# Optimization experiments

Measured on AMD Instinct MI355X. Metric: run time of the kernel, lower is better.

The kernel has to match this reference:

```python
import jax, jax.numpy as jnp
import numpy as np

B, S, D, H = 8, 256, 16, 256
NH, DH, L = 8, H // 8, 3
H2, H4, FF = H // 2, H // 4, 2 * H


def _ln(x, g, b, eps=1e-5):
    m = jnp.mean(x, axis=-1, keepdims=True)
    v = jnp.var(x, axis=-1, keepdims=True)
    return (x - m) / jnp.sqrt(v + eps) * g + b


def setup_inputs() -> dict:
    key = jax.random.key(0)
    ks = iter(jax.random.split(key, 32))
    w = lambda *sh: jax.random.normal(next(ks), sh, jnp.float32) * 0.05
    inp = {
        'parts': jax.random.normal(next(ks), (B, S, D), jnp.float32),
        'target_sequence': jax.random.randint(next(ks), (B, S), 0, S),
        # part encoder
        'W_pe1': w(H2, D), 'b_pe1': jnp.zeros((H2,)),
        'W_pe2': w(H2, H2), 'b_pe2': jnp.zeros((H2,)),
        'pos_emb': w(S, H4),
        # transformer encoder (3 layers, stacked)
        'Wqkv': w(L, 3 * H, H), 'bqkv': jnp.zeros((L, 3 * H)),
        'Wo': w(L, H, H), 'bo': jnp.zeros((L, H)),
        'ln1_g': jnp.ones((L, H)), 'ln1_b': jnp.zeros((L, H)),
        'W1f': w(L, FF, H), 'b1f': jnp.zeros((L, FF)),
        'W2f': w(L, H, FF), 'b2f': jnp.zeros((L, H)),
        'ln2_g': jnp.ones((L, H)), 'ln2_b': jnp.zeros((L, H)),
        # LSTM decoder
        'Wih': w(4 * H, H), 'Whh': w(4 * H, H),
        'bih': jnp.zeros((4 * H,)), 'bhh': jnp.zeros((4 * H,)),
        # pointer
        'Wp': w(H, H), 'bp': jnp.zeros((H,)), 'v_ptr': w(H),
    }
    return inp


def reference(parts, target_sequence, W_pe1, b_pe1, W_pe2, b_pe2, pos_emb,
              Wqkv, bqkv, Wo, bo, ln1_g, ln1_b, W1f, b1f, W2f, b2f, ln2_g, ln2_b,
              Wih, Whh, bih, bhh, Wp, bp, v_ptr):
    Bk, Sk = parts.shape[:2]
    # ---- encode_inputs (dropout inactive in eval) ----
    pe = jax.nn.relu(parts @ W_pe1.T + b_pe1) @ W_pe2.T + b_pe2          # [B,S,H/2]
    pos = jnp.broadcast_to(pos_emb[None, :Sk], (Bk, Sk, H4))              # [B,S,H/4]
    pad = jnp.zeros((Bk, Sk, H - H2 - H4), parts.dtype)
    x = jnp.concatenate([pe, pos, pad], axis=-1)                          # [B,S,H]
    scale = 1.0 / np.sqrt(DH)
    for l in range(L):  # post-norm transformer encoder layers
        qkv = x @ Wqkv[l].T + bqkv[l]
        q, k, v = jnp.split(qkv, 3, axis=-1)
        q = q.reshape(Bk, Sk, NH, DH)
        k = k.reshape(Bk, Sk, NH, DH)
        v = v.reshape(Bk, Sk, NH, DH)
        att = jax.nn.softmax(jnp.einsum('bqhd,bkhd->bhqk', q, k) * scale, axis=-1)
        o = jnp.einsum('bhqk,bkhd->bqhd', att, v).reshape(Bk, Sk, H)
        o = o @ Wo[l].T + bo[l]
        x = _ln(x + o, ln1_g[l], ln1_b[l])
        f = jax.nn.relu(x @ W1f[l].T + b1f[l]) @ W2f[l].T + b2f[l]
        x = _ln(x + f, ln2_g[l], ln2_b[l])
    enc = x                                                               # [B,S,H]
    # ---- teacher-forced LSTM decode (teacher_forcing_ratio=1.0) ----
    gathered = jnp.take_along_axis(enc, target_sequence[:, :, None], axis=1)  # [B,T,H]
    dec_in = jnp.concatenate([jnp.zeros((Bk, 1, H), enc.dtype), gathered[:, :-1]], 1)
    dec_in = dec_in.transpose(1, 0, 2)                                    # [T,B,H]

    def step(carry, xt):
        h, c = carry
        g = xt @ Wih.T + bih + h @ Whh.T + bhh
        i, f, gg, o = jnp.split(g, 4, axis=-1)
        c = jax.nn.sigmoid(f) * c + jax.nn.sigmoid(i) * jnp.tanh(gg)
        h = jax.nn.sigmoid(o) * jnp.tanh(c)
        return (h, c), h

    h0 = jnp.zeros((Bk, H), enc.dtype)
    _, dec_out = jax.lax.scan(step, (h0, h0), dec_in)
    dec_out = dec_out.transpose(1, 0, 2)                                  # [B,T,H]
    # ---- pointer logits: v . tanh(Wp d_t + Wp e_i), batched over (t,i) ----
    pd = dec_out @ Wp.T + bp                                              # [B,T,H]
    pen = enc @ Wp.T + bp                                                 # [B,S,H]
    logits = jnp.tanh(pd[:, :, None, :] + pen[:, None, :, :]) @ v_ptr     # [B,T,S]
    return logits
```

## Files before the change

kernel.cpp:

```cpp
#include <hip/hip_runtime.h>
#include <cstdint>
#include <cstddef>


typedef _Float16 h2 __attribute__((ext_vector_type(2)));
typedef short bf16x8 __attribute__((ext_vector_type(8)));
typedef float f32x4 __attribute__((ext_vector_type(4)));

__device__ __forceinline__ float sigf(float x) { return 1.0f / (1.0f + __expf(-x)); }
__device__ __forceinline__ float tanhfast(float x) {
  float e = __expf(-2.0f * fabsf(x));
  float t = (1.0f - e) / (1.0f + e);
  return copysignf(t, x);
}
__device__ __forceinline__ h2 cvt2(float a, float b) {
  h2 r; r.x = (_Float16)a; r.y = (_Float16)b; return r;
}
__device__ __forceinline__ h2 bch2(unsigned int u) { return __builtin_bit_cast(h2, u); }
__device__ __forceinline__ unsigned int bcu(h2 v) { return __builtin_bit_cast(unsigned int, v); }
__device__ __forceinline__ unsigned short f2bf(float f) {
  unsigned int u = __float_as_uint(f);
  u = (u + 0x7fffu + ((u >> 16) & 1u)) >> 16;
  return (unsigned short)u;
}

__device__ __forceinline__ float fdot2f(h2 a, h2 b, float c) {
#if __has_builtin(__builtin_amdgcn_fdot2)
  return __builtin_amdgcn_fdot2(a, b, c, false);
#else
  return fmaf((float)a.x, (float)b.x, fmaf((float)a.y, (float)b.y, c));
#endif
}

__global__ void convert_all(const float* __restrict__ s0, ushort* __restrict__ d0,
                            const float* __restrict__ s1, ushort* __restrict__ d1,
                            const float* __restrict__ s2, ushort* __restrict__ d2,
                            const float* __restrict__ s3, ushort* __restrict__ d3,
                            const float* __restrict__ s4, ushort* __restrict__ d4,
                            const float* __restrict__ s5, ushort* __restrict__ d5) {
  int i = blockIdx.x * 256 + threadIdx.x;
  if (i < 589824) { d0[i] = f2bf(s0[i]); return; }
  i -= 589824;
  if (i < 196608) { d1[i] = f2bf(s1[i]); return; }
  i -= 196608;
  if (i < 393216) { d2[i] = f2bf(s2[i]); return; }
  i -= 393216;
  if (i < 393216) { d3[i] = f2bf(s3[i]); return; }
  i -= 393216;
  if (i < 262144) { d4[i] = f2bf(s4[i]); return; }
  i -= 262144;
  if (i < 65536) d5[i] = f2bf(s5[i]);
}

__global__ void part_encoder(const float* __restrict__ parts, const float* __restrict__ Wpe1,
                             const float* __restrict__ bpe1, const float* __restrict__ Wpe2,
                             const float* __restrict__ bpe2, const float* __restrict__ pos,
                             float* __restrict__ x, ushort* __restrict__ xb) {
  __shared__ float prow[16];
  __shared__ float pe1[128];
  int row = blockIdx.x;
  int s = row & 255;
  int tid = threadIdx.x;
  if (tid < 16) prow[tid] = parts[row * 16 + tid];
  __syncthreads();
  float a = bpe1[tid];
#pragma unroll
  for (int k = 0; k < 16; ++k) a = fmaf(prow[k], Wpe1[tid * 16 + k], a);
  pe1[tid] = fmaxf(a, 0.0f);
  __syncthreads();
  float a2 = bpe2[tid];
  for (int k = 0; k < 128; ++k) a2 = fmaf(pe1[k], Wpe2[tid * 128 + k], a2);
  x[(size_t)row * 256 + tid] = a2;
  xb[(size_t)row * 256 + tid] = f2bf(a2);
  if (tid < 64) {
    float p = pos[s * 64 + tid];
    x[(size_t)row * 256 + 128 + tid] = p;
    xb[(size_t)row * 256 + 128 + tid] = f2bf(p);
    x[(size_t)row * 256 + 192 + tid] = 0.0f;
    xb[(size_t)row * 256 + 192 + tid] = 0;
  }
}

template <int ACT, int OUT>
__global__ __launch_bounds__(64) void gemm_bf16(
    const ushort* __restrict__ A, const ushort* __restrict__ Wt,
    const float* __restrict__ bias1, const float* __restrict__ bias2,
    void* __restrict__ Cout, int N, int K) {
  int lane = threadIdx.x;
  int m0 = blockIdx.y * 16;
  int n0 = blockIdx.x * 64;
  int r15 = lane & 15;
  int kg = lane >> 4;
  f32x4 acc0 = {0.f, 0.f, 0.f, 0.f}, acc1 = acc0, acc2 = acc0, acc3 = acc0;
  const ushort* arow = A + (size_t)(m0 + r15) * K + kg * 8;
  const ushort* w0 = Wt + (size_t)(n0 + r15) * K + kg * 8;
  const ushort* w1 = w0 + (size_t)16 * K;
  const ushort* w2 = w0 + (size_t)32 * K;
  const ushort* w3 = w0 + (size_t)48 * K;
  for (int k0 = 0; k0 < K; k0 += 32) {
    bf16x8 af = *(const bf16x8*)(arow + k0);
    bf16x8 b0 = *(const bf16x8*)(w0 + k0);
    bf16x8 b1 = *(const bf16x8*)(w1 + k0);
    bf16x8 b2 = *(const bf16x8*)(w2 + k0);
    bf16x8 b3 = *(const bf16x8*)(w3 + k0);
    acc0 = __builtin_amdgcn_mfma_f32_16x16x32_bf16(af, b0, acc0, 0, 0, 0);
    acc1 = __builtin_amdgcn_mfma_f32_16x16x32_bf16(af, b1, acc1, 0, 0, 0);
    acc2 = __builtin_amdgcn_mfma_f32_16x16x32_bf16(af, b2, acc2, 0, 0, 0);
    acc3 = __builtin_amdgcn_mfma_f32_16x16x32_bf16(af, b3, acc3, 0, 0, 0);
  }
#pragma unroll
  for (int nn = 0; nn < 4; ++nn) {
    f32x4 a = (nn == 0) ? acc0 : (nn == 1) ? acc1 : (nn == 2) ? acc2 : acc3;
    int n = n0 + nn * 16 + r15;
    float bsum = bias1[n] + (bias2 ? bias2[n] : 0.0f);
    if (OUT == 3) {
      int b = m0 >> 8;
      int mloc = (m0 & 255) + kg * 4;
      float4 o4 = {a[0] + bsum, a[1] + bsum, a[2] + bsum, a[3] + bsum};
      *(float4*)&((float*)Cout)[((size_t)(b * 256 + n)) * 256 + mloc] = o4;
    } else {
#pragma unroll
      for (int r = 0; r < 4; ++r) {
        int m = m0 + kg * 4 + r;
        float v = a[r] + bsum;
        if (ACT == 1) v = fmaxf(v, 0.0f);
        if (OUT == 1)
          ((ushort*)Cout)[(size_t)m * N + n] = f2bf(v);
        else
          ((float*)Cout)[(size_t)m * N + n] = v;
      }
    }
  }
}

__global__ void attn_kernel(const float* __restrict__ qkv, ushort* __restrict__ attout) {
  extern __shared__ float sm[];
  float* kl = sm;
  float* ql = sm + 256 * 33;
  float* sc = sm + 256 * 33 + 32 * 33;
  int qt = blockIdx.x, h = blockIdx.y, b = blockIdx.z;
  int tid = threadIdx.x;
  {
    int j = tid;
    const float* src = qkv + (size_t)(b * 256 + j) * 768 + 256 + h * 32;
#pragma unroll
    for (int d = 0; d < 32; d += 4) {
      float4 v = *(const float4*)(src + d);
      kl[j * 33 + d] = v.x; kl[j * 33 + d + 1] = v.y; kl[j * 33 + d + 2] = v.z; kl[j * 33 + d + 3] = v.w;
    }
  }
  {
    int i = tid >> 3, d4 = (tid & 7) * 4;
    const float* src = qkv + (size_t)(b * 256 + qt * 32 + i) * 768 + h * 32;
    float4 v = *(const float4*)(src + d4);
    ql[i * 33 + d4] = v.x; ql[i * 33 + d4 + 1] = v.y; ql[i * 33 + d4 + 2] = v.z; ql[i * 33 + d4 + 3] = v.w;
  }
  __syncthreads();
  int i = tid >> 3, c = tid & 7;
  const float scale = 0.17677669529663687f;
  float sv[32];
  float mx = -1e30f;
  for (int jj = 0; jj < 32; ++jj) {
    int j = jj * 8 + c;
    float s = 0.0f;
#pragma unroll
    for (int d = 0; d < 32; ++d) s = fmaf(ql[i * 33 + d], kl[j * 33 + d], s);
    s *= scale;
    sv[jj] = s;
    mx = fmaxf(mx, s);
  }
  mx = fmaxf(mx, __shfl_xor(mx, 1));
  mx = fmaxf(mx, __shfl_xor(mx, 2));
  mx = fmaxf(mx, __shfl_xor(mx, 4));
  float sum = 0.0f;
  for (int jj = 0; jj < 32; ++jj) {
    float p = __expf(sv[jj] - mx);
    sc[i * 257 + jj * 8 + c] = p;
    sum += p;
  }
  sum += __shfl_xor(sum, 1);
  sum += __shfl_xor(sum, 2);
  sum += __shfl_xor(sum, 4);
  float inv = 1.0f / sum;
  __syncthreads();
  float a0 = 0, a1 = 0, a2 = 0, a3 = 0;
  int d0 = c * 4;
  const float* vbase = qkv + 512 + h * 32 + d0;
  for (int j = 0; j < 256; ++j) {
    float p = sc[i * 257 + j];
    float4 v = *(const float4*)(vbase + (size_t)(b * 256 + j) * 768);
    a0 = fmaf(p, v.x, a0); a1 = fmaf(p, v.y, a1); a2 = fmaf(p, v.z, a2); a3 = fmaf(p, v.w, a3);
  }
  int orow = b * 256 + qt * 32 + i;
  ushort4 o4;
  o4.x = f2bf(a0 * inv); o4.y = f2bf(a1 * inv); o4.z = f2bf(a2 * inv); o4.w = f2bf(a3 * inv);
  *(ushort4*)&attout[(size_t)orow * 256 + h * 32 + d0] = o4;
}

__global__ void ln_residual(float* __restrict__ x, const float* __restrict__ o,
                            const float* __restrict__ g, const float* __restrict__ bt,
                            ushort* __restrict__ xb) {
  int row = blockIdx.x, tid = threadIdx.x;
  float e = x[(size_t)row * 256 + tid] + o[(size_t)row * 256 + tid];
  float s = e, q = e * e;
#pragma unroll
  for (int off = 32; off >= 1; off >>= 1) {
    s += __shfl_xor(s, off);
    q += __shfl_xor(q, off);
  }
  __shared__ float ps[4], pq[4];
  int wid = tid >> 6, lane = tid & 63;
  if (lane == 0) { ps[wid] = s; pq[wid] = q; }
  __syncthreads();
  float St = ps[0] + ps[1] + ps[2] + ps[3];
  float Qt = pq[0] + pq[1] + pq[2] + pq[3];
  float mean = St * (1.0f / 256.0f);
  float var = Qt * (1.0f / 256.0f) - mean * mean;
  float y = (e - mean) * rsqrtf(var + 1e-5f) * g[tid] + bt[tid];
  x[(size_t)row * 256 + tid] = y;
  xb[(size_t)row * 256 + tid] = f2bf(y);
}

__global__ void gather_dec_in(const ushort* __restrict__ encb, const int* __restrict__ ts,
                              ushort* __restrict__ dec_in) {
  int bx = blockIdx.x;
  int t = bx >> 3, b = bx & 7;
  int tid = threadIdx.x;
  ushort4 v = {0, 0, 0, 0};
  if (t > 0) {
    int sidx = ts[b * 256 + t - 1];
    v = *(const ushort4*)&encb[((size_t)(b * 256 + sidx)) * 256 + tid * 4];
  }
  *(ushort4*)&dec_in[(size_t)bx * 256 + tid * 4] = v;
}

__global__ __attribute__((amdgpu_flat_work_group_size(512, 512), amdgpu_waves_per_eu(1, 1)))
void lstm_scan512(const float* __restrict__ Xw, const float* __restrict__ Whh,
                  ushort* __restrict__ dec_out) {
  extern __shared__ char smem[];
  uint4* wlds = (uint4*)smem;
  h2* hbuf = (h2*)(smem + 131072);
  int b = blockIdx.x;
  int t0 = threadIdx.x;
  int u = t0 >> 1, p = t0 & 1;
  int rA = u + 256 * p;
  int rB = u + 512 + 256 * p;

  h2 w0[96], w1[96];
  {
    const float4* sA = (const float4*)(Whh + (size_t)rA * 256);
    const float4* sB = (const float4*)(Whh + (size_t)rB * 256);
#pragma unroll
    for (int k = 0; k < 48; ++k) {
      float4 v = sA[k];
      w0[2 * k] = cvt2(v.x, v.y);
      w0[2 * k + 1] = cvt2(v.z, v.w);
    }
#pragma unroll
    for (int k = 0; k < 48; ++k) {
      float4 v = sB[k];
      w1[2 * k] = cvt2(v.x, v.y);
      w1[2 * k + 1] = cvt2(v.z, v.w);
    }
#pragma unroll
    for (int qc = 0; qc < 8; ++qc) {
      float4 vA0 = sA[48 + 2 * qc], vA1 = sA[48 + 2 * qc + 1];
      float4 vB0 = sB[48 + 2 * qc], vB1 = sB[48 + 2 * qc + 1];
      uint4 uA, uB;
      uA.x = bcu(cvt2(vA0.x, vA0.y)); uA.y = bcu(cvt2(vA0.z, vA0.w));
      uA.z = bcu(cvt2(vA1.x, vA1.y)); uA.w = bcu(cvt2(vA1.z, vA1.w));
      uB.x = bcu(cvt2(vB0.x, vB0.y)); uB.y = bcu(cvt2(vB0.z, vB0.w));
      uB.z = bcu(cvt2(vB1.x, vB1.y)); uB.w = bcu(cvt2(vB1.z, vB1.w));
      wlds[qc * 1024 + rA] = uA;
      wlds[qc * 1024 + rB] = uB;
    }
  }
  if (t0 < 128) ((uint4*)hbuf)[t0 & 63] = make_uint4(0, 0, 0, 0);
  float c = 0.0f;
  float xnA = Xw[(size_t)b * 1024 + rA];
  float xnB = Xw[(size_t)b * 1024 + rB];
  __syncthreads();

  for (int t = 0; t < 256; ++t) {
    float xwA = xnA, xwB = xnB;
    if (t < 255) {
      const float* xp = Xw + (size_t)((t + 1) * 8 + b) * 1024;
      xnA = xp[rA]; xnB = xp[rB];
    }
    const uint4* hb = (const uint4*)(hbuf + (size_t)(t & 1) * 128);
    float a0 = 0.0f, a1 = 0.0f;
#pragma unroll
    for (int q = 0; q < 24; ++q) {
      uint4 hv = hb[q];
      h2 hx = bch2(hv.x), hy = bch2(hv.y), hz = bch2(hv.z), hw = bch2(hv.w);
      a0 = fdot2f(w0[4 * q], hx, a0); a0 = fdot2f(w0[4 * q + 1], hy, a0);
      a0 = fdot2f(w0[4 * q + 2], hz, a0); a0 = fdot2f(w0[4 * q + 3], hw, a0);
      a1 = fdot2f(w1[4 * q], hx, a1); a1 = fdot2f(w1[4 * q + 1], hy, a1);
      a1 = fdot2f(w1[4 * q + 2], hz, a1); a1 = fdot2f(w1[4 * q + 3], hw, a1);
    }
#pragma unroll
    for (int qc = 0; qc < 8; ++qc) {
      uint4 hv = hb[24 + qc];
      h2 hx = bch2(hv.x), hy = bch2(hv.y), hz = bch2(hv.z), hw = bch2(hv.w);
      uint4 uA = wlds[qc * 1024 + rA];
      uint4 uB = wlds[qc * 1024 + rB];
      a0 = fdot2f(bch2(uA.x), hx, a0); a0 = fdot2f(bch2(uA.y), hy, a0);
      a0 = fdot2f(bch2(uA.z), hz, a0); a0 = fdot2f(bch2(uA.w), hw, a0);
      a1 = fdot2f(bch2(uB.x), hx, a1); a1 = fdot2f(bch2(uB.y), hy, a1);
      a1 = fdot2f(bch2(uB.z), hz, a1); a1 = fdot2f(bch2(uB.w), hw, a1);
    }
    a0 += xwA;
    a1 += xwB;
    float ev = sigf(a0) * tanhfast(a1);
    float ep = __shfl_xor(ev, 1);
    if (p == 1) {
      c = sigf(a0) * c + ep;
      float hv_ = sigf(a1) * tanhfast(c);
      ((_Float16*)(hbuf + (size_t)((t + 1) & 1) * 128))[u] = (_Float16)hv_;
      dec_out[((size_t)(b * 256 + t)) * 256 + u] = f2bf(hv_);
    }
    __syncthreads();
  }
}

__global__ void pointer_kernel(const float* __restrict__ pd, const float* __restrict__ penT,
                               const float* __restrict__ vptr, float* __restrict__ out) {
  __shared__ float pdr[256];
  __shared__ float vl[256];
  int bx = blockIdx.x;
  int b = bx >> 8;
  int tid = threadIdx.x;
  pdr[tid] = pd[(size_t)bx * 256 + tid];
  vl[tid] = vptr[tid];
  __syncthreads();
  const float* pT = penT + (size_t)b * 256 * 256;
  float acc = 0.0f;
  for (int h = 0; h < 256; ++h) {
    acc = fmaf(vl[h], tanhfast(pdr[h] + pT[(size_t)h * 256 + tid]), acc);
  }
  out[(size_t)bx * 256 + tid] = acc;
}

extern "C" void kernel_launch(void* const* d_in, const int* in_sizes, int n_in,
                              void* d_out, int out_size, void* d_ws, size_t ws_size,
                              hipStream_t stream) {
  const float* parts = (const float*)d_in[0];
  const int* ts = (const int*)d_in[1];
  const float* Wpe1 = (const float*)d_in[2];
  const float* bpe1 = (const float*)d_in[3];
  const float* Wpe2 = (const float*)d_in[4];
  const float* bpe2 = (const float*)d_in[5];
  const float* pos = (const float*)d_in[6];
  const float* Wqkv = (const float*)d_in[7];
  const float* bqkv = (const float*)d_in[8];
  const float* Wo = (const float*)d_in[9];
  const float* bo = (const float*)d_in[10];
  const float* ln1g = (const float*)d_in[11];
  const float* ln1b = (const float*)d_in[12];
  const float* W1f = (const float*)d_in[13];
  const float* b1f = (const float*)d_in[14];
  const float* W2f = (const float*)d_in[15];
  const float* b2f = (const float*)d_in[16];
  const float* ln2g = (const float*)d_in[17];
  const float* ln2b = (const float*)d_in[18];
  const float* Wih = (const float*)d_in[19];
  const float* Whh = (const float*)d_in[20];
  const float* bih = (const float*)d_in[21];
  const float* bhh = (const float*)d_in[22];
  const float* Wp = (const float*)d_in[23];
  const float* bp = (const float*)d_in[24];
  const float* vptr = (const float*)d_in[25];
  float* out = (float*)d_out;

  float* W = (float*)d_ws;
  float* xbuf = W;
  ushort* xbf = (ushort*)(W + 524288);
  float* SCR = W + 786432;
  float* qkvb = SCR;
  float* obuf = SCR + 1572864;
  float* Xw = SCR;
  float* pdb = SCR;
  float* penTb = SCR + 1048576;
  ushort* attbf = (ushort*)(W + 2883584);
  ushort* ffbf = (ushort*)(W + 3145728);
  ushort* dec_inbf = (ushort*)(W + 3145728);
  ushort* dec_outbf = (ushort*)(W + 3407872);
  ushort* wqkvbf = (ushort*)(W + 3670016);
  ushort* wobf   = (ushort*)(W + 3964928);
  ushort* w1fbf  = (ushort*)(W + 4063232);
  ushort* w2fbf  = (ushort*)(W + 4259840);
  ushort* wihbf  = (ushort*)(W + 4456448);
  ushort* wpbf   = (ushort*)(W + 4587520);

  const int attnLDS = (256 * 33 + 32 * 33 + 32 * 257) * 4;
  const int scan512LDS = 131072 + 1024;
  hipFuncSetAttribute((const void*)attn_kernel, hipFuncAttributeMaxDynamicSharedMemorySize, attnLDS);
  hipFuncSetAttribute((const void*)lstm_scan512, hipFuncAttributeMaxDynamicSharedMemorySize, scan512LDS);

  convert_all<<<7424, 256, 0, stream>>>(Wqkv, wqkvbf, Wo, wobf, W1f, w1fbf,
                                        W2f, w2fbf, Wih, wihbf, Wp, wpbf);

  part_encoder<<<2048, 128, 0, stream>>>(parts, Wpe1, bpe1, Wpe2, bpe2, pos, xbuf, xbf);
  for (int l = 0; l < 3; ++l) {
    gemm_bf16<0, 0><<<dim3(12, 128), 64, 0, stream>>>(xbf, wqkvbf + (size_t)l * 196608,
                                                      bqkv + l * 768, nullptr, qkvb, 768, 256);
    attn_kernel<<<dim3(8, 8, 8), 256, attnLDS, stream>>>(qkvb, attbf);
    gemm_bf16<0, 0><<<dim3(4, 128), 64, 0, stream>>>(attbf, wobf + (size_t)l * 65536,
                                                     bo + l * 256, nullptr, obuf, 256, 256);
    ln_residual<<<2048, 256, 0, stream>>>(xbuf, obuf, ln1g + l * 256, ln1b + l * 256, xbf);
    gemm_bf16<1, 1><<<dim3(8, 128), 64, 0, stream>>>(xbf, w1fbf + (size_t)l * 131072,
                                                     b1f + l * 512, nullptr, ffbf, 512, 256);
    gemm_bf16<0, 0><<<dim3(4, 128), 64, 0, stream>>>(ffbf, w2fbf + (size_t)l * 131072,
                                                     b2f + l * 256, nullptr, obuf, 256, 512);
    ln_residual<<<2048, 256, 0, stream>>>(xbuf, obuf, ln2g + l * 256, ln2b + l * 256, xbf);
  }
  gather_dec_in<<<2048, 64, 0, stream>>>(xbf, ts, dec_inbf);
  gemm_bf16<0, 0><<<dim3(16, 128), 64, 0, stream>>>(dec_inbf, wihbf, bih, bhh, Xw, 1024, 256);
  lstm_scan512<<<8, 512, scan512LDS, stream>>>(Xw, Whh, dec_outbf);
  gemm_bf16<0, 0><<<dim3(4, 128), 64, 0, stream>>>(dec_outbf, wpbf, bp, nullptr, pdb, 256, 256);
  gemm_bf16<0, 3><<<dim3(4, 128), 64, 0, stream>>>(xbf, wpbf, bp, nullptr, penTb, 256, 256);
  pointer_kernel<<<2048, 256, 0, stream>>>(pdb, penTb, vptr, out);
}
```

Baseline: 825.5 us.

## Fuse residual LayerNorm into output GEMMs and gather into LSTM input GEMM

Adds a gemm_ln kernel in which four waves compute a full 16x256 output tile, stage it in shared memory, then apply the residual add and LayerNorm before writing fp32 and bf16 activations. This replaces the separate Wo/W2f GEMM plus ln_residual launches and the obuf round trip. The teacher-forcing gather is also folded into the Wih GEMM's A-row addressing through the ts indices, which removes the gather_dec_in kernel and the dec_in buffer. The trade-off is that the fused GEMM grid drops to 128 blocks of 256 threads, which lowers parallelism for those GEMMs.

```diff
diff --git a/kernel.cpp b/kernel.cpp
--- a/kernel.cpp
+++ b/kernel.cpp
@@ -81,16 +81,83 @@
   }
 }
 
-template <int ACT, int OUT>
+template <int ACT, int OUT, int GATHER>
 __global__ __launch_bounds__(64) void gemm_bf16(
     const ushort* __restrict__ A, const ushort* __restrict__ Wt,
     const float* __restrict__ bias1, const float* __restrict__ bias2,
-    void* __restrict__ Cout, int N, int K) {
+    void* __restrict__ Cout, int N, int K, const int* __restrict__ ts) {
   int lane = threadIdx.x;
   int m0 = blockIdx.y * 16;
   int n0 = blockIdx.x * 64;
   int r15 = lane & 15;
   int kg = lane >> 4;
+  f32x4 acc0 = {0.f, 0.f, 0.f, 0.f}, acc1 = acc0, acc2 = acc0, acc3 = acc0;
+  const ushort* arow;
+  bool zeroA = false;
+  if (GATHER) {
+    int m = m0 + r15;
+    int t = m >> 3, b = m & 7;
+    if (t == 0) { zeroA = true; arow = A; }
+    else {
+      int sidx = ts[b * 256 + t - 1];
+      arow = A + (size_t)(b * 256 + sidx) * 256 + kg * 8;
+    }
+  } else {
+    arow = A + (size_t)(m0 + r15) * K + kg * 8;
+  }
+  const ushort* w0 = Wt + (size_t)(n0 + r15) * K + kg * 8;
+  const ushort* w1 = w0 + (size_t)16 * K;
+  const ushort* w2 = w0 + (size_t)32 * K;
+  const ushort* w3 = w0 + (size_t)48 * K;
+  for (int k0 = 0; k0 < K; k0 += 32) {
+    bf16x8 af;
+    if (GATHER && zeroA) af = (bf16x8){0, 0, 0, 0, 0, 0, 0, 0};
+    else af = *(const bf16x8*)(arow + k0);
+    bf16x8 b0 = *(const bf16x8*)(w0 + k0);
+    bf16x8 b1 = *(const bf16x8*)(w1 + k0);
+    bf16x8 b2 = *(const bf16x8*)(w2 + k0);
+    bf16x8 b3 = *(const bf16x8*)(w3 + k0);
+    acc0 = __builtin_amdgcn_mfma_f32_16x16x32_bf16(af, b0, acc0, 0, 0, 0);
+    acc1 = __builtin_amdgcn_mfma_f32_16x16x32_bf16(af, b1, acc1, 0, 0, 0);
+    acc2 = __builtin_amdgcn_mfma_f32_16x16x32_bf16(af, b2, acc2, 0, 0, 0);
+    acc3 = __builtin_amdgcn_mfma_f32_16x16x32_bf16(af, b3, acc3, 0, 0, 0);
+  }
+#pragma unroll
+  for (int nn = 0; nn < 4; ++nn) {
+    f32x4 a = (nn == 0) ? acc0 : (nn == 1) ? acc1 : (nn == 2) ? acc2 : acc3;
+    int n = n0 + nn * 16 + r15;
+    float bsum = bias1[n] + (bias2 ? bias2[n] : 0.0f);
+    if (OUT == 3) {
+      int b = m0 >> 8;
+      int mloc = (m0 & 255) + kg * 4;
+      float4 o4 = {a[0] + bsum, a[1] + bsum, a[2] + bsum, a[3] + bsum};
+      *(float4*)&((float*)Cout)[((size_t)(b * 256 + n)) * 256 + mloc] = o4;
+    } else {
+#pragma unroll
+      for (int r = 0; r < 4; ++r) {
+        int m = m0 + kg * 4 + r;
+        float v = a[r] + bsum;
+        if (ACT == 1) v = fmaxf(v, 0.0f);
+        if (OUT == 1)
+          ((ushort*)Cout)[(size_t)m * N + n] = f2bf(v);
+        else
+          ((float*)Cout)[(size_t)m * N + n] = v;
+      }
+    }
+  }
+}
+
+__global__ __launch_bounds__(256) void gemm_ln(
+    const ushort* __restrict__ A, const ushort* __restrict__ Wt,
+    const float* __restrict__ bias1, float* __restrict__ x,
+    const float* __restrict__ g, const float* __restrict__ bt,
+    ushort* __restrict__ xb, int K) {
+  __shared__ float osm[16][257];
+  int tid = threadIdx.x;
+  int w = tid >> 6, lane = tid & 63;
+  int m0 = blockIdx.x * 16;
+  int n0 = w * 64;
+  int r15 = lane & 15, kg = lane >> 4;
   f32x4 acc0 = {0.f, 0.f, 0.f, 0.f}, acc1 = acc0, acc2 = acc0, acc3 = acc0;
   const ushort* arow = A + (size_t)(m0 + r15) * K + kg * 8;
   const ushort* w0 = Wt + (size_t)(n0 + r15) * K + kg * 8;
@@ -111,26 +178,71 @@
 #pragma unroll
   for (int nn = 0; nn < 4; ++nn) {
     f32x4 a = (nn == 0) ? acc0 : (nn == 1) ? acc1 : (nn == 2) ? acc2 : acc3;
-    int n = n0 + nn * 16 + r15;
-    float bsum = bias1[n] + (bias2 ? bias2[n] : 0.0f);
-    if (OUT == 3) {
-      int b = m0 >> 8;
-      int mloc = (m0 & 255) + kg * 4;
-      float4 o4 = {a[0] + bsum, a[1] + bsum, a[2] + bsum, a[3] + bsum};
-      *(float4*)&((float*)Cout)[((size_t)(b * 256 + n)) * 256 + mloc] = o4;
-    } else {
-#pragma unroll
-      for (int r = 0; r < 4; ++r) {
-        int m = m0 + kg * 4 + r;
-        float v = a[r] + bsum;
-        if (ACT == 1) v = fmaxf(v, 0.0f);
-        if (OUT == 1)
-          ((ushort*)Cout)[(size_t)m * N + n] = f2bf(v);
-        else
-          ((float*)Cout)[(size_t)m * N + n] = v;
-      }
-    }
-  }
+    int col = n0 + nn * 16 + r15;
+    float bsum = bias1[col];
+#pragma unroll
+    for (int r = 0; r < 4; ++r) osm[kg * 4 + r][col] = a[r] + bsum;
+  }
+  __syncthreads();
+  int row = tid >> 4, j = tid & 15;
+  size_t xoff = (size_t)(m0 + row) * 256 + j * 16;
+  float4 xv0 = *(const float4*)&x[xoff];
+  float4 xv1 = *(const float4*)&x[xoff + 4];
+  float4 xv2 = *(const float4*)&x[xoff + 8];
+  float4 xv3 = *(const float4*)&x[xoff + 12];
+  float e0 = xv0.x + osm[row][j * 16 + 0], e1 = xv0.y + osm[row][j * 16 + 1];
+  float e2 = xv0.z + osm[row][j * 16 + 2], e3 = xv0.w + osm[row][j * 16 + 3];
+  float e4 = xv1.x + osm[row][j * 16 + 4], e5 = xv1.y + osm[row][j * 16 + 5];
+  float e6 = xv1.z + osm[row][j * 16 + 6], e7 = xv1.w + osm[row][j * 16 + 7];
+  float e8 = xv2.x + osm[row][j * 16 + 8], e9 = xv2.y + osm[row][j * 16 + 9];
+  float e10 = xv2.z + osm[row][j * 16 + 10], e11 = xv2.w + osm[row][j * 16 + 11];
+  float e12 = xv3.x + osm[row][j * 16 + 12], e13 = xv3.y + osm[row][j * 16 + 13];
+  float e14 = xv3.z + osm[row][j * 16 + 14], e15 = xv3.w + osm[row][j * 16 + 15];
+  float s = ((e0 + e1) + (e2 + e3)) + ((e4 + e5) + (e6 + e7)) +
+            ((e8 + e9) + (e10 + e11)) + ((e12 + e13) + (e14 + e15));
+  float q = ((e0 * e0 + e1 * e1) + (e2 * e2 + e3 * e3)) +
+            ((e4 * e4 + e5 * e5) + (e6 * e6 + e7 * e7)) +
+            ((e8 * e8 + e9 * e9) + (e10 * e10 + e11 * e11)) +
+            ((e12 * e12 + e13 * e13) + (e14 * e14 + e15 * e15));
+#pragma unroll
+  for (int off = 1; off <= 8; off <<= 1) {
+    s += __shfl_xor(s, off);
+    q += __shfl_xor(q, off);
+  }
+  float mean = s * (1.0f / 256.0f);
+  float var = q * (1.0f / 256.0f) - mean * mean;
+  float inv = rsqrtf(var + 1e-5f);
+  const float* gp = g + j * 16;
+  const float* bp2 = bt + j * 16;
+  float y0 = (e0 - mean) * inv * gp[0] + bp2[0];
+  float y1 = (e1 - mean) * inv * gp[1] + bp2[1];
+  float y2 = (e2 - mean) * inv * gp[2] + bp2[2];
+  float y3 = (e3 - mean) * inv * gp[3] + bp2[3];
+  float y4 = (e4 - mean) * inv * gp[4] + bp2[4];
+  float y5 = (e5 - mean) * inv * gp[5] + bp2[5];
+  float y6 = (e6 - mean) * inv * gp[6] + bp2[6];
+  float y7 = (e7 - mean) * inv * gp[7] + bp2[7];
+  float y8 = (e8 - mean) * inv * gp[8] + bp2[8];
+  float y9 = (e9 - mean) * inv * gp[9] + bp2[9];
+  float y10 = (e10 - mean) * inv * gp[10] + bp2[10];
+  float y11 = (e11 - mean) * inv * gp[11] + bp2[11];
+  float y12 = (e12 - mean) * inv * gp[12] + bp2[12];
+  float y13 = (e13 - mean) * inv * gp[13] + bp2[13];
+  float y14 = (e14 - mean) * inv * gp[14] + bp2[14];
+  float y15 = (e15 - mean) * inv * gp[15] + bp2[15];
+  *(float4*)&x[xoff] = make_float4(y0, y1, y2, y3);
+  *(float4*)&x[xoff + 4] = make_float4(y4, y5, y6, y7);
+  *(float4*)&x[xoff + 8] = make_float4(y8, y9, y10, y11);
+  *(float4*)&x[xoff + 12] = make_float4(y12, y13, y14, y15);
+  ushort4 u0, u1, u2, u3;
+  u0.x = f2bf(y0); u0.y = f2bf(y1); u0.z = f2bf(y2); u0.w = f2bf(y3);
+  u1.x = f2bf(y4); u1.y = f2bf(y5); u1.z = f2bf(y6); u1.w = f2bf(y7);
+  u2.x = f2bf(y8); u2.y = f2bf(y9); u2.z = f2bf(y10); u2.w = f2bf(y11);
+  u3.x = f2bf(y12); u3.y = f2bf(y13); u3.z = f2bf(y14); u3.w = f2bf(y15);
+  *(ushort4*)&xb[xoff] = u0;
+  *(ushort4*)&xb[xoff + 4] = u1;
+  *(ushort4*)&xb[xoff + 8] = u2;
+  *(ushort4*)&xb[xoff + 12] = u3;
 }
 
 __global__ void attn_kernel(const float* __restrict__ qkv, ushort* __restrict__ attout) {
@@ -195,43 +307,6 @@
   ushort4 o4;
   o4.x = f2bf(a0 * inv); o4.y = f2bf(a1 * inv); o4.z = f2bf(a2 * inv); o4.w = f2bf(a3 * inv);
   *(ushort4*)&attout[(size_t)orow * 256 + h * 32 + d0] = o4;
-}
-
-__global__ void ln_residual(float* __restrict__ x, const float* __restrict__ o,
-                            const float* __restrict__ g, const float* __restrict__ bt,
-                            ushort* __restrict__ xb) {
-  int row = blockIdx.x, tid = threadIdx.x;
-  float e = x[(size_t)row * 256 + tid] + o[(size_t)row * 256 + tid];
-  float s = e, q = e * e;
-#pragma unroll
-  for (int off = 32; off >= 1; off >>= 1) {
-    s += __shfl_xor(s, off);
-    q += __shfl_xor(q, off);
-  }
-  __shared__ float ps[4], pq[4];
-  int wid = tid >> 6, lane = tid & 63;
-  if (lane == 0) { ps[wid] = s; pq[wid] = q; }
-  __syncthreads();
-  float St = ps[0] + ps[1] + ps[2] + ps[3];
-  float Qt = pq[0] + pq[1] + pq[2] + pq[3];
-  float mean = St * (1.0f / 256.0f);
-  float var = Qt * (1.0f / 256.0f) - mean * mean;
-  float y = (e - mean) * rsqrtf(var + 1e-5f) * g[tid] + bt[tid];
-  x[(size_t)row * 256 + tid] = y;
-  xb[(size_t)row * 256 + tid] = f2bf(y);
-}
-
-__global__ void gather_dec_in(const ushort* __restrict__ encb, const int* __restrict__ ts,
-                              ushort* __restrict__ dec_in) {
-  int bx = blockIdx.x;
-  int t = bx >> 3, b = bx & 7;
-  int tid = threadIdx.x;
-  ushort4 v = {0, 0, 0, 0};
-  if (t > 0) {
-    int sidx = ts[b * 256 + t - 1];
-    v = *(const ushort4*)&encb[((size_t)(b * 256 + sidx)) * 256 + tid * 4];
-  }
-  *(ushort4*)&dec_in[(size_t)bx * 256 + tid * 4] = v;
 }
 
 __global__ __attribute__((amdgpu_flat_work_group_size(512, 512), amdgpu_waves_per_eu(1, 1)))
@@ -377,13 +452,11 @@
   ushort* xbf = (ushort*)(W + 524288);
   float* SCR = W + 786432;
   float* qkvb = SCR;
-  float* obuf = SCR + 1572864;
   float* Xw = SCR;
   float* pdb = SCR;
   float* penTb = SCR + 1048576;
   ushort* attbf = (ushort*)(W + 2883584);
   ushort* ffbf = (ushort*)(W + 3145728);
-  ushort* dec_inbf = (ushort*)(W + 3145728);
   ushort* dec_outbf = (ushort*)(W + 3407872);
   ushort* wqkvbf = (ushort*)(W + 3670016);
   ushort* wobf   = (ushort*)(W + 3964928);
@@ -402,22 +475,22 @@
 
   part_encoder<<<2048, 128, 0, stream>>>(parts, Wpe1, bpe1, Wpe2, bpe2, pos, xbuf, xbf);
   for (int l = 0; l < 3; ++l) {
-    gemm_bf16<0, 0><<<dim3(12, 128), 64, 0, stream>>>(xbf, wqkvbf + (size_t)l * 196608,
-                                                      bqkv + l * 768, nullptr, qkvb, 768, 256);
+    gemm_bf16<0, 0, 0><<<dim3(12, 128), 64, 0, stream>>>(
+        xbf, wqkvbf + (size_t)l * 196608, bqkv + l * 768, nullptr, qkvb, 768, 256, nullptr);
     attn_kernel<<<dim3(8, 8, 8), 256, attnLDS, stream>>>(qkvb, attbf);
-    gemm_bf16<0, 0><<<dim3(4, 128), 64, 0, stream>>>(attbf, wobf + (size_t)l * 65536,
-                                                     bo + l * 256, nullptr, obuf, 256, 256);
-    ln_residual<<<2048, 256, 0, stream>>>(xbuf, obuf, ln1g + l * 256, ln1b + l * 256, xbf);
-    gemm_bf16<1, 1><<<dim3(8, 128), 64, 0, stream>>>(xbf, w1fbf + (size_t)l * 131072,
-                                                     b1f + l * 512, nullptr, ffbf, 512, 256);
-    gemm_bf16<0, 0><<<dim3(4, 128), 64, 0, stream>>>(ffbf, w2fbf + (size_t)l * 131072,
-                                                     b2f + l * 256, nullptr, obuf, 256, 512);
-    ln_residual<<<2048, 256, 0, stream>>>(xbuf, obuf, ln2g + l * 256, ln2b + l * 256, xbf);
-  }
-  gather_dec_in<<<2048, 64, 0, stream>>>(xbf, ts, dec_inbf);
-  gemm_bf16<0, 0><<<dim3(16, 128), 64, 0, stream>>>(dec_inbf, wihbf, bih, bhh, Xw, 1024, 256);
+    gemm_ln<<<128, 256, 0, stream>>>(attbf, wobf + (size_t)l * 65536, bo + l * 256,
+                                     xbuf, ln1g + l * 256, ln1b + l * 256, xbf, 256);
+    gemm_bf16<1, 1, 0><<<dim3(8, 128), 64, 0, stream>>>(
+        xbf, w1fbf + (size_t)l * 131072, b1f + l * 512, nullptr, ffbf, 512, 256, nullptr);
+    gemm_ln<<<128, 256, 0, stream>>>(ffbf, w2fbf + (size_t)l * 131072, b2f + l * 256,
+                                     xbuf, ln2g + l * 256, ln2b + l * 256, xbf, 512);
+  }
+  gemm_bf16<0, 0, 1><<<dim3(16, 128), 64, 0, stream>>>(
+      xbf, wihbf, bih, bhh, Xw, 1024, 256, ts);
   lstm_scan512<<<8, 512, scan512LDS, stream>>>(Xw, Whh, dec_outbf);
-  gemm_bf16<0, 0><<<dim3(4, 128), 64, 0, stream>>>(dec_outbf, wpbf, bp, nullptr, pdb, 256, 256);
-  gemm_bf16<0, 3><<<dim3(4, 128), 64, 0, stream>>>(xbf, wpbf, bp, nullptr, penTb, 256, 256);
+  gemm_bf16<0, 0, 0><<<dim3(4, 128), 64, 0, stream>>>(
+      dec_outbf, wpbf, bp, nullptr, pdb, 256, 256, nullptr);
+  gemm_bf16<0, 3, 0><<<dim3(4, 128), 64, 0, stream>>>(
+      xbf, wpbf, bp, nullptr, penTb, 256, 256, nullptr);
   pointer_kernel<<<2048, 256, 0, stream>>>(pdb, penTb, vptr, out);
 }
```

Result: no change. 826.9 us (+0.2%).
